# Kernel optimization log

Hardware: AMD Instinct MI355X
Metric: run time of the kernel (lower is better)

Reference implementation:

```python
import jax, jax.numpy as jnp
import numpy as np

ITER_NUM = 3       # nSteps of the SICE proximal loop (module iterNum)
NS_ITERS = 7       # Newton-Schulz iterations, hardcoded in _sice
F_LR = 5.0         # sice_lrate
F_SPARSITY = 0.07  # sparsity_val
BN_EPS = 1e-5


def _inv_sqrtm(x, iterN):
    """Batched Newton-Schulz inverse matrix square root (Sqrtm.forward)."""
    d = x.shape[-1]
    I3 = 3.0 * jnp.eye(d, dtype=x.dtype)
    normA = jnp.trace(x, axis1=-2, axis2=-1)            # [B]
    A = x / normA[:, None, None]
    ZY = 0.5 * (I3 - A)
    Y = A @ ZY
    Z = ZY
    for _ in range(iterN - 2):
        ZY = 0.5 * (I3 - Z @ Y)
        Y = Y @ ZY
        Z = ZY @ Z
    ZYZ = 0.5 * (I3 - Z @ Y) @ Z
    return ZYZ * (normA ** -0.5)[:, None, None]


def _covpool(x):
    """x: [B,C,H,W] -> centered second-order pooling [B,C,C] (Covpool)."""
    b, c, h, w = x.shape
    m = h * w
    xf = x.reshape(b, c, m)
    xc = xf - xf.mean(axis=-1, keepdims=True)
    # x @ I_hat @ x^T == (x - mean)(x - mean)^T / M
    return (xc @ xc.transpose(0, 2, 1)) / m


def _sice(x, jitter):
    C = _covpool(x)
    C = C / jnp.trace(C, axis1=-2, axis2=-1)[:, None, None]
    Ij = jnp.diag(1e-10 + 1e-9 * jitter)[None].astype(C.dtype)   # [1,D,D]
    zz = _inv_sqrtm(C + Ij, NS_ITERS)
    LLT = zz @ zz                                                # inv covariance init
    sym_C = 0.5 * (C + C.transpose(0, 2, 1))
    for i in range(ITER_NUM):
        Lp = jax.nn.relu(LLT)
        Lm = jax.nn.relu(-LLT)
        zz = _inv_sqrtm(LLT + Ij, NS_ITERS)
        g12 = -(zz @ zz) + sym_C
        dec = F_LR * (1.0 - i / (ITER_NUM - 1.0))
        Lp = jax.nn.relu(Lp - dec * (g12 + F_SPARSITY))
        Lm = jax.nn.relu(Lm - dec * (-g12 + F_SPARSITY))
        LLT = Lp - Lm
        LLT = 0.5 * (LLT + LLT.transpose(0, 2, 1))
    return LLT / jnp.sqrt(jnp.trace(LLT, axis1=-2, axis2=-1))[:, None, None]


def reference(x, conv_w, gamma, beta, jitter):
    # 1x1 conv dimension reduction + BatchNorm (batch stats, train mode) + ReLU
    y = jnp.einsum('bchw,dc->bdhw', x, conv_w)
    mu = y.mean(axis=(0, 2, 3), keepdims=True)
    var = y.var(axis=(0, 2, 3), keepdims=True)
    y = (y - mu) / jnp.sqrt(var + BN_EPS)
    y = jax.nn.relu(y * gamma[None, :, None, None] + beta[None, :, None, None])
    out = _sice(y, jitter)                                       # [B,D,D]
    b, d = out.shape[0], out.shape[1]
    iu = np.nonzero(np.triu(np.ones((d, d))).reshape(-1))[0]     # Triuvec indices
    return out.reshape(b, d * d)[:, iu]                          # [B, D*(D+1)/2]


def setup_inputs() -> dict:
    key = jax.random.key(0)
    k1, k2, k3 = jax.random.split(key, 3)
    B, CIN, H, W, DR = 32, 2048, 28, 28, 256
    x = jax.random.normal(k1, (B, CIN, H, W), dtype=jnp.float32)
    # kaiming normal, mode=fan_out (fan_out = DR*1*1): std = sqrt(2/DR)
    conv_w = jax.random.normal(k2, (DR, CIN), dtype=jnp.float32) * np.sqrt(2.0 / DR).astype(np.float32)
    gamma = jnp.ones((DR,), dtype=jnp.float32)
    beta = jnp.zeros((DR,), dtype=jnp.float32)
    jitter = jax.random.uniform(k3, (DR,), dtype=jnp.float32)
    return {"x": x, "conv_w": conv_w, "gamma": gamma, "beta": beta, "jitter": jitter}
```

## Files before the change

kernel.cpp:

```cpp
#include <hip/hip_runtime.h>
#include <utility>


typedef unsigned short u16;
typedef __attribute__((ext_vector_type(8))) __bf16 bf16x8;
typedef __attribute__((ext_vector_type(8))) _Float16 f16x8;
typedef __attribute__((ext_vector_type(4))) float f32x4;

#define DEV __device__ __forceinline__

DEV u16 f2bf(float f) {
  unsigned x = __float_as_uint(f);
  x += 0x7fffu + ((x >> 16) & 1u);
  return (u16)(x >> 16);
}
DEV float bf2f(u16 h) { return __uint_as_float(((unsigned)h) << 16); }

#define SB_SUM   0
#define SB_SSQ   256
#define SB_IJ    512
#define SB_TRC   768
#define SB_TR2   800
#define SB_TR3   832
#define SB_TRL   864
#define SB_DEN   896
#define SB_IJSUM 928

__global__ __launch_bounds__(256) void k_prep(const float* __restrict__ w,
                                              const float* __restrict__ jitter,
                                              _Float16* __restrict__ w_half,
                                              float* __restrict__ sb) {
  int gid = blockIdx.x * 256 + threadIdx.x;
  if (gid < 256 * 2048) w_half[gid] = (_Float16)w[gid];
  if (blockIdx.x == 0) {
    int t = threadIdx.x;
    sb[SB_SUM + t] = 0.f;
    sb[SB_SSQ + t] = 0.f;
    float ij = 1e-10f + 1e-9f * jitter[t];
    sb[SB_IJ + t] = ij;
    if (t < 160) sb[SB_TRC + t] = 0.f;
    __shared__ float red[256];
    red[t] = ij; __syncthreads();
    for (int off = 128; off > 0; off >>= 1) {
      if (t < off) red[t] += red[t + off];
      __syncthreads();
    }
    if (t == 0) sb[SB_IJSUM] = red[0];
  }
}

__global__ __launch_bounds__(256) void k_xt(const float* __restrict__ x,
                                            _Float16* __restrict__ xt) {
  int ht = blockIdx.x;
  int ct = blockIdx.y;
  int b = blockIdx.z;
  int t = threadIdx.x;
  __shared__ _Float16 ls[64 * 68];
  int hw0 = ht * 64, c0 = ct * 64;
  const float* xb = x + ((size_t)b * 2048 + c0) * 784;
#pragma unroll
  for (int it = 0; it < 4; ++it) {
    int cc = (t >> 4) + it * 16;
    int s = t & 15;
    int hw = hw0 + s * 4;
    float4 v = make_float4(0.f, 0.f, 0.f, 0.f);
    if (hw < 784) v = *(const float4*)(xb + (size_t)cc * 784 + hw);
    _Float16* d = &ls[cc * 68 + s * 4];
    d[0] = (_Float16)v.x; d[1] = (_Float16)v.y;
    d[2] = (_Float16)v.z; d[3] = (_Float16)v.w;
  }
  __syncthreads();
#pragma unroll
  for (int it = 0; it < 2; ++it) {
    int idx = t + it * 256;
    int hwr = idx >> 3, s8 = idx & 7;
    if (hw0 + hwr < 784) {
      union { _Float16 h[8]; uint4 v; } pk;
#pragma unroll
      for (int cc = 0; cc < 8; ++cc) pk.h[cc] = ls[(s8 * 8 + cc) * 68 + hwr];
      *(uint4*)(xt + ((size_t)b * 784 + hw0 + hwr) * 2048 + c0 + s8 * 8) = pk.v;
    }
  }
}

__global__ __launch_bounds__(256) void k_conv(const _Float16* __restrict__ w_half,
                                              const _Float16* __restrict__ xt,
                                              _Float16* __restrict__ y,
                                              float* __restrict__ sb) {
  int xb = blockIdx.x;
  int ht = xb >> 5, b = xb & 31;
  int t = threadIdx.x;
  int wv = t >> 6, lane = t & 63, m = lane & 15, quad = lane >> 4;
  __shared__ _Float16 lsA[256 * 40];
  __shared__ _Float16 lsB[32 * 40];
  int hw0 = ht * 32;
  f32x4 acc[4][2];
#pragma unroll
  for (int i = 0; i < 4; ++i)
#pragma unroll
    for (int j = 0; j < 2; ++j) acc[i][j] = (f32x4){0.f, 0.f, 0.f, 0.f};
  int rowA = t >> 2, segA = t & 3;
  const _Float16* wp = w_half + (size_t)rowA * 2048 + segA * 8;
  bool doB = (t < 128);
  int hw = hw0 + rowA;
  const _Float16* xp = xt + ((size_t)b * 784 + hw) * 2048 + segA * 8;
  uint4 ra0, ra1, ra2, ra3, rb;
  ra0 = *(const uint4*)(wp);
  ra1 = *(const uint4*)(wp + 64 * 2048);
  ra2 = *(const uint4*)(wp + 128 * 2048);
  ra3 = *(const uint4*)(wp + 192 * 2048);
  rb = (uint4){0u, 0u, 0u, 0u};
  if (doB && hw < 784) rb = *(const uint4*)(xp);
  for (int kc = 0; kc < 64; ++kc) {
    int lo = rowA * 40 + segA * 8;
    *(uint4*)&lsA[lo] = ra0;
    *(uint4*)&lsA[lo + 64 * 40] = ra1;
    *(uint4*)&lsA[lo + 128 * 40] = ra2;
    *(uint4*)&lsA[lo + 192 * 40] = ra3;
    if (doB) *(uint4*)&lsB[lo] = rb;
    __syncthreads();
    if (kc < 63) {
      int k0 = (kc + 1) * 32;
      ra0 = *(const uint4*)(wp + k0);
      ra1 = *(const uint4*)(wp + 64 * 2048 + k0);
      ra2 = *(const uint4*)(wp + 128 * 2048 + k0);
      ra3 = *(const uint4*)(wp + 192 * 2048 + k0);
      rb = (uint4){0u, 0u, 0u, 0u};
      if (doB && hw < 784) rb = *(const uint4*)(xp + k0);
    }
    f16x8 af[4], bfg[2];
#pragma unroll
    for (int i = 0; i < 4; ++i)
      af[i] = *(const f16x8*)&lsA[(wv * 64 + i * 16 + m) * 40 + quad * 8];
#pragma unroll
    for (int j = 0; j < 2; ++j)
      bfg[j] = *(const f16x8*)&lsB[(j * 16 + m) * 40 + quad * 8];
#pragma unroll
    for (int i = 0; i < 4; ++i)
#pragma unroll
      for (int j = 0; j < 2; ++j)
        acc[i][j] = __builtin_amdgcn_mfma_f32_16x16x32_f16(af[i], bfg[j], acc[i][j], 0, 0, 0);
    __syncthreads();
  }
  float* sum = sb + SB_SUM;
  float* ssq = sb + SB_SSQ;
#pragma unroll
  for (int i = 0; i < 4; ++i) {
#pragma unroll
    for (int r = 0; r < 4; ++r) {
      float s = 0.f, q = 0.f;
#pragma unroll
      for (int j = 0; j < 2; ++j) {
        float v = acc[i][j][r];
        s += v; q += v * v;
      }
      s += __shfl_xor(s, 1); s += __shfl_xor(s, 2);
      s += __shfl_xor(s, 4); s += __shfl_xor(s, 8);
      q += __shfl_xor(q, 1); q += __shfl_xor(q, 2);
      q += __shfl_xor(q, 4); q += __shfl_xor(q, 8);
      if (m == 0) {
        int R = wv * 64 + i * 16 + quad * 4 + r;
        atomicAdd(&sum[R], s);
        atomicAdd(&ssq[R], q);
      }
    }
  }
#pragma unroll
  for (int i = 0; i < 4; ++i)
#pragma unroll
    for (int j = 0; j < 2; ++j)
#pragma unroll
      for (int r = 0; r < 4; ++r) {
        int R = wv * 64 + i * 16 + quad * 4 + r;
        int hwc = hw0 + j * 16 + m;
        if (hwc < 784) y[((size_t)b * 256 + R) * 784 + hwc] = (_Float16)acc[i][j][r];
      }
}

__global__ __launch_bounds__(256) void k_bnapply(const _Float16* __restrict__ y,
                                                 const float* __restrict__ gamma,
                                                 const float* __restrict__ beta,
                                                 const float* __restrict__ sb,
                                                 _Float16* __restrict__ yc) {
  int xb = blockIdx.x;
  int d = xb >> 5, b = xb & 31, t = threadIdx.x;
  float mu = sb[SB_SUM + d] * (1.0f / 25088.0f);
  float var = sb[SB_SSQ + d] * (1.0f / 25088.0f) - mu * mu;
  float sc = gamma[d] / sqrtf(var + 1e-5f);
  float sh = beta[d] - mu * sc;
  const _Float16* row = y + ((size_t)b * 256 + d) * 784;
  float v[4];
  float s = 0.f;
#pragma unroll
  for (int i = 0; i < 4; ++i) {
    int idx = t + i * 256;
    float u = 0.f;
    if (idx < 784) u = fmaxf((float)row[idx] * sc + sh, 0.f);
    v[i] = u; s += u;
  }
  __shared__ float red[256];
  red[t] = s; __syncthreads();
  for (int off = 128; off > 0; off >>= 1) {
    if (t < off) red[t] += red[t + off];
    __syncthreads();
  }
  float mean = red[0] * (1.0f / 784.0f);
  _Float16* out = yc + ((size_t)b * 256 + d) * 800;
#pragma unroll
  for (int i = 0; i < 4; ++i) {
    int idx = t + i * 256;
    if (idx < 784) out[idx] = (_Float16)(v[i] - mean);
  }
  if (t < 16) out[784 + t] = (_Float16)0.f;
}

__global__ __launch_bounds__(256) void k_gram(const _Float16* __restrict__ yc,
                                              float* __restrict__ C,
                                              float* __restrict__ sb) {
  int xb = blockIdx.x;
  int tile = xb >> 5, b = xb & 31;
  int tr = tile >> 2, tc = tile & 3;
  int t = threadIdx.x, wv = t >> 6, lane = t & 63, m = lane & 15, quad = lane >> 4;
  int wr = (wv >> 1) * 32, wc = (wv & 1) * 32;
  __shared__ _Float16 lsA[64 * 40], lsB[64 * 40];
  f32x4 acc[2][2];
#pragma unroll
  for (int i = 0; i < 2; ++i)
#pragma unroll
    for (int j = 0; j < 2; ++j) acc[i][j] = (f32x4){0.f, 0.f, 0.f, 0.f};
  int row = t >> 2, seg = t & 3;
  const _Float16* Ap = yc + ((size_t)b * 256 + tr * 64 + row) * 800 + seg * 8;
  const _Float16* Bp = yc + ((size_t)b * 256 + tc * 64 + row) * 800 + seg * 8;
  uint4 rA = *(const uint4*)(Ap);
  uint4 rB = *(const uint4*)(Bp);
  for (int kc = 0; kc < 25; ++kc) {
    int lo = row * 40 + seg * 8;
    *(uint4*)&lsA[lo] = rA;
    *(uint4*)&lsB[lo] = rB;
    __syncthreads();
    if (kc < 24) {
      int k0 = (kc + 1) * 32;
      rA = *(const uint4*)(Ap + k0);
      rB = *(const uint4*)(Bp + k0);
    }
    f16x8 a0 = *(const f16x8*)&lsA[(wr + m) * 40 + quad * 8];
    f16x8 a1 = *(const f16x8*)&lsA[(wr + 16 + m) * 40 + quad * 8];
    f16x8 b0 = *(const f16x8*)&lsB[(wc + m) * 40 + quad * 8];
    f16x8 b1 = *(const f16x8*)&lsB[(wc + 16 + m) * 40 + quad * 8];
    acc[0][0] = __builtin_amdgcn_mfma_f32_16x16x32_f16(a0, b0, acc[0][0], 0, 0, 0);
    acc[0][1] = __builtin_amdgcn_mfma_f32_16x16x32_f16(a0, b1, acc[0][1], 0, 0, 0);
    acc[1][0] = __builtin_amdgcn_mfma_f32_16x16x32_f16(a1, b0, acc[1][0], 0, 0, 0);
    acc[1][1] = __builtin_amdgcn_mfma_f32_16x16x32_f16(a1, b1, acc[1][1], 0, 0, 0);
    __syncthreads();
  }
  const float inv = 1.0f / 784.0f;
#pragma unroll
  for (int i = 0; i < 2; ++i)
#pragma unroll
    for (int j = 0; j < 2; ++j)
#pragma unroll
      for (int r = 0; r < 4; ++r) {
        int R = tr * 64 + wr + i * 16 + quad * 4 + r;
        int Cc = tc * 64 + wc + j * 16 + m;
        float v = acc[i][j][r] * inv;
        C[((size_t)b * 256 + R) * 256 + Cc] = v;
        if (R == Cc) atomicAdd(&sb[SB_TRC + b], v);
      }
}

__global__ __launch_bounds__(256) void k_prepAZY(const float* __restrict__ src,
                                                 float* __restrict__ symC,
                                                 u16* __restrict__ Ah, u16* __restrict__ Al,
                                                 u16* __restrict__ ZYh, u16* __restrict__ ZYl,
                                                 float* __restrict__ sb, int slot, int mode) {
  int xb = blockIdx.x;
  int i = xb >> 5, b = xb & 31, j = threadIdx.x;
  float trv = (mode == 0) ? 1.0f : sb[slot + b];
  float denom = trv + sb[SB_IJSUM];
  if (i == 0 && j == 0) sb[SB_DEN + b] = denom;
  size_t idx = ((size_t)b * 256 + i) * 256 + j;
  float v;
  if (mode == 0) {
    float trC = sb[SB_TRC + b];
    float vij = src[idx] / trC;
    float vji = src[((size_t)b * 256 + j) * 256 + i] / trC;
    symC[idx] = 0.5f * (vij + vji);
    v = vij;
  } else {
    v = src[idx];
  }
  if (i == j) v += sb[SB_IJ + i];
  float A = v / denom;
  u16 h = f2bf(A);
  Ah[idx] = h; Al[idx] = f2bf(A - bf2f(h));
  float zy = 0.5f * ((i == j ? 3.0f : 0.0f) - A);
  h = f2bf(zy);
  ZYh[idx] = h; ZYl[idx] = f2bf(zy - bf2f(h));
}

struct MMArgs {
  const u16* Ah; const u16* Al; const u16* Bh; const u16* Bl;
  u16* Oh; u16* Ol; float* Of; float* tr; int emode;
};

__global__ __launch_bounds__(256) void mm_ns(MMArgs g0, MMArgs g1,
                                             const float* __restrict__ sb) {
  int xb = blockIdx.x;
  int b = xb & 31;
  int rest = xb >> 5;
  MMArgs g = (rest < 16) ? g0 : g1;
  int tile = rest & 15;
  int tr = tile >> 2, tc = tile & 3;
  int t = threadIdx.x, wv = t >> 6, lane = t & 63, m = lane & 15, quad = lane >> 4;
  int wr = (wv >> 1) * 32, wc = (wv & 1) * 32;
  __shared__ u16 lsAh[64 * 40], lsAl[64 * 40], lsBh[64 * 40], lsBl[64 * 40];
  f32x4 acc[2][2];
#pragma unroll
  for (int i = 0; i < 2; ++i)
#pragma unroll
    for (int j = 0; j < 2; ++j) acc[i][j] = (f32x4){0.f, 0.f, 0.f, 0.f};
  int row = t >> 2, seg = t & 3;
  size_t aoff = ((size_t)b * 256 + tr * 64 + row) * 256 + seg * 8;
  size_t boff = ((size_t)b * 256 + tc * 64 + row) * 256 + seg * 8;
  uint4 rAh = *(const uint4*)(g.Ah + aoff);
  uint4 rAl = *(const uint4*)(g.Al + aoff);
  uint4 rBh = *(const uint4*)(g.Bh + boff);
  uint4 rBl = *(const uint4*)(g.Bl + boff);
  for (int kc = 0; kc < 8; ++kc) {
    int lo = row * 40 + seg * 8;
    *(uint4*)&lsAh[lo] = rAh;
    *(uint4*)&lsAl[lo] = rAl;
    *(uint4*)&lsBh[lo] = rBh;
    *(uint4*)&lsBl[lo] = rBl;
    __syncthreads();
    if (kc < 7) {
      int k0 = (kc + 1) * 32;
      rAh = *(const uint4*)(g.Ah + aoff + k0);
      rAl = *(const uint4*)(g.Al + aoff + k0);
      rBh = *(const uint4*)(g.Bh + boff + k0);
      rBl = *(const uint4*)(g.Bl + boff + k0);
    }
    bf16x8 ah[2], al[2], bh[2], bl[2];
#pragma unroll
    for (int i = 0; i < 2; ++i) {
      ah[i] = *(const bf16x8*)&lsAh[(wr + i * 16 + m) * 40 + quad * 8];
      al[i] = *(const bf16x8*)&lsAl[(wr + i * 16 + m) * 40 + quad * 8];
      bh[i] = *(const bf16x8*)&lsBh[(wc + i * 16 + m) * 40 + quad * 8];
      bl[i] = *(const bf16x8*)&lsBl[(wc + i * 16 + m) * 40 + quad * 8];
    }
#pragma unroll
    for (int i = 0; i < 2; ++i)
#pragma unroll
      for (int j = 0; j < 2; ++j) {
        acc[i][j] = __builtin_amdgcn_mfma_f32_16x16x32_bf16(ah[i], bh[j], acc[i][j], 0, 0, 0);
        acc[i][j] = __builtin_amdgcn_mfma_f32_16x16x32_bf16(ah[i], bl[j], acc[i][j], 0, 0, 0);
        acc[i][j] = __builtin_amdgcn_mfma_f32_16x16x32_bf16(al[i], bh[j], acc[i][j], 0, 0, 0);
      }
    __syncthreads();
  }
  float scl = 1.0f;
  if (g.emode == 2) scl = 1.0f / sqrtf(sb[SB_DEN + b]);
#pragma unroll
  for (int i = 0; i < 2; ++i)
#pragma unroll
    for (int j = 0; j < 2; ++j)
#pragma unroll
      for (int r = 0; r < 4; ++r) {
        int R = tr * 64 + wr + i * 16 + quad * 4 + r;
        int Cc = tc * 64 + wc + j * 16 + m;
        float v = acc[i][j][r];
        if (g.emode == 1) v = 0.5f * ((R == Cc ? 3.0f : 0.0f) - v);
        else if (g.emode == 2) v = v * scl;
        size_t oidx = ((size_t)b * 256 + R) * 256 + Cc;
        if (g.emode == 3) {
          g.Of[oidx] = v;
          if (R == Cc && g.tr) atomicAdd(g.tr + b, v);
        } else {
          u16 h = f2bf(v);
          g.Oh[oidx] = h;
          g.Ol[oidx] = f2bf(v - bf2f(h));
        }
      }
}

__global__ __launch_bounds__(256) void k_sice(const float* __restrict__ LLT,
                                              const float* __restrict__ P,
                                              const float* __restrict__ symC,
                                              float* __restrict__ out,
                                              float* __restrict__ sb, int slot,
                                              float dec) {
  int xb = blockIdx.x;
  int b = xb & 31, p = xb >> 5;
  const int TRt[10] = {0, 0, 0, 0, 1, 1, 1, 2, 2, 3};
  const int TCt[10] = {0, 1, 2, 3, 1, 2, 3, 2, 3, 3};
  int tr = TRt[p], tc = TCt[p];
  __shared__ float ft[64][65];
  __shared__ float ot[64][65];
  int t = threadIdx.x;
  size_t base = (size_t)b * 65536;
#pragma unroll 4
  for (int it = 0; it < 16; ++it) {
    int idx = it * 256 + t;
    int r = idx >> 6, c = idx & 63;
    size_t o = base + (size_t)(tc * 64 + r) * 256 + tr * 64 + c;
    float L = LLT[o];
    float g = symC[o] - P[o];
    float f = fmaxf(fmaxf(L, 0.f) - dec * (g + 0.07f), 0.f) -
              fmaxf(fmaxf(-L, 0.f) - dec * (-g + 0.07f), 0.f);
    ft[r][c] = f;
  }
  __syncthreads();
  float tsum = 0.f;
#pragma unroll 4
  for (int it = 0; it < 16; ++it) {
    int idx = it * 256 + t;
    int r = idx >> 6, c = idx & 63;
    size_t o = base + (size_t)(tr * 64 + r) * 256 + tc * 64 + c;
    float L = LLT[o];
    float g = symC[o] - P[o];
    float f = fmaxf(fmaxf(L, 0.f) - dec * (g + 0.07f), 0.f) -
              fmaxf(fmaxf(-L, 0.f) - dec * (-g + 0.07f), 0.f);
    float val = 0.5f * (f + ft[c][r]);
    out[o] = val;
    ot[r][c] = val;
    if (tr == tc && r == c) tsum += val;
  }
  if (tr == tc) {
    if (tsum != 0.f) atomicAdd(&sb[slot + b], tsum);
  } else {
    __syncthreads();
#pragma unroll 4
    for (int it = 0; it < 16; ++it) {
      int idx = it * 256 + t;
      int r = idx >> 6, c = idx & 63;
      size_t o = base + (size_t)(tc * 64 + r) * 256 + tr * 64 + c;
      out[o] = ot[c][r];
    }
  }
}

__global__ __launch_bounds__(256) void k_out(const float* __restrict__ LLT,
                                             const float* __restrict__ sb,
                                             float* __restrict__ out) {
  int xb = blockIdx.x;
  int i = xb >> 5, b = xb & 31, j = threadIdx.x;
  if (j < i) return;
  float inv = 1.0f / sqrtf(sb[SB_TRL + b]);
  int tl = i * 256 - (i * (i - 1)) / 2 + (j - i);
  out[(size_t)b * 32896 + tl] = LLT[((size_t)b * 256 + i) * 256 + j] * inv;
}

extern "C" void kernel_launch(void* const* d_in, const int* in_sizes, int n_in,
                              void* d_out, int out_size, void* d_ws, size_t ws_size,
                              hipStream_t stream) {
  const float* x = (const float*)d_in[0];
  const float* w = (const float*)d_in[1];
  const float* gamma = (const float*)d_in[2];
  const float* beta = (const float*)d_in[3];
  const float* jitter = (const float*)d_in[4];
  char* ws = (char*)d_ws;

  _Float16* w_half = (_Float16*)(ws + 0);
  float* sb = (float*)(ws + (1 << 20));
  _Float16* y = (_Float16*)(ws + (2 << 20));
  _Float16* yc = (_Float16*)(ws + (16 << 20));
  _Float16* xt = (_Float16*)(ws + (32 << 20));
  char* ov = ws + (32 << 20);
  float* Craw = (float*)(ov + 0);
  float* symC = (float*)(ov + 8388608);
  float* LLTa = (float*)(ov + 16777216);
  float* P = (float*)(ov + 25165824);
  float* LLTb = (float*)(ov + 33554432);
  u16* bf[12];
  for (int i = 0; i < 12; ++i) bf[i] = (u16*)(ov + 41943040 + (size_t)i * 4194304);

  k_prep<<<2048, 256, 0, stream>>>(w, jitter, w_half, sb);
  k_xt<<<dim3(13, 32, 32), 256, 0, stream>>>(x, xt);
  k_conv<<<800, 256, 0, stream>>>(w_half, xt, y, sb);
  k_bnapply<<<8192, 256, 0, stream>>>(y, gamma, beta, sb, yc);
  k_gram<<<512, 256, 0, stream>>>(yc, Craw, sb);

  auto run_ns = [&](const float* src, int mode, int slot_in, float* Pout,
                    float* tr_out) {
    k_prepAZY<<<8192, 256, 0, stream>>>(src, symC, bf[0], bf[1], bf[2], bf[3], sb, slot_in, mode);
    u16 *Ah = bf[0], *Al = bf[1], *ZYh = bf[2], *ZYl = bf[3];
    u16 *Yh = bf[4], *Yl = bf[5], *Z2h = bf[6], *Z2l = bf[7];
    u16 *Th = bf[8], *Tl = bf[9], *zzh = bf[10], *zzl = bf[11];
    MMArgs m1{Ah, Al, ZYh, ZYl, Yh, Yl, nullptr, nullptr, 0};
    mm_ns<<<512, 256, 0, stream>>>(m1, m1, sb);
    u16 *Ych = Yh, *Ycl = Yl, *Yah = Ah, *Yal = Al;
    u16 *Zch = ZYh, *Zcl = ZYl, *Zah = Z2h, *Zal = Z2l;
    for (int it = 0; it < 5; ++it) {
      MMArgs mt{Zch, Zcl, Ych, Ycl, Th, Tl, nullptr, nullptr, 1};
      mm_ns<<<512, 256, 0, stream>>>(mt, mt, sb);
      MMArgs my{Ych, Ycl, Th, Tl, Yah, Yal, nullptr, nullptr, 0};
      MMArgs mz{Th, Tl, Zch, Zcl, Zah, Zal, nullptr, nullptr, 0};
      mm_ns<<<1024, 256, 0, stream>>>(my, mz, sb);
      std::swap(Ych, Yah); std::swap(Ycl, Yal);
      std::swap(Zch, Zah); std::swap(Zcl, Zal);
    }
    MMArgs mt6{Zch, Zcl, Ych, Ycl, Th, Tl, nullptr, nullptr, 1};
    mm_ns<<<512, 256, 0, stream>>>(mt6, mt6, sb);
    MMArgs mz7{Th, Tl, Zch, Zcl, zzh, zzl, nullptr, nullptr, 2};
    mm_ns<<<512, 256, 0, stream>>>(mz7, mz7, sb);
    MMArgs mzz{zzh, zzl, zzh, zzl, nullptr, nullptr, Pout, tr_out, 3};
    mm_ns<<<512, 256, 0, stream>>>(mzz, mzz, sb);
  };

  run_ns(Craw, 0, 0, LLTa, sb + SB_TR2);
  run_ns(LLTa, 1, SB_TR2, P, nullptr);
  k_sice<<<320, 256, 0, stream>>>(LLTa, P, symC, LLTb, sb, SB_TR3, 5.0f);
  run_ns(LLTb, 1, SB_TR3, P, nullptr);
  k_sice<<<320, 256, 0, stream>>>(LLTb, P, symC, LLTa, sb, SB_TRL, 2.5f);

  k_out<<<8192, 256, 0, stream>>>(LLTa, sb, (float*)d_out);
}
```

Measured before the change: 1.019 ms.

## Fuse input transpose into conv and drop LDS staging in gram and NS matmuls

```diff
diff --git a/kernel.cpp b/kernel.cpp
--- a/kernel.cpp
+++ b/kernel.cpp
@@ -49,92 +49,63 @@
   }
 }
 
-__global__ __launch_bounds__(256) void k_xt(const float* __restrict__ x,
-                                            _Float16* __restrict__ xt) {
-  int ht = blockIdx.x;
-  int ct = blockIdx.y;
-  int b = blockIdx.z;
-  int t = threadIdx.x;
-  __shared__ _Float16 ls[64 * 68];
-  int hw0 = ht * 64, c0 = ct * 64;
-  const float* xb = x + ((size_t)b * 2048 + c0) * 784;
-#pragma unroll
-  for (int it = 0; it < 4; ++it) {
-    int cc = (t >> 4) + it * 16;
-    int s = t & 15;
-    int hw = hw0 + s * 4;
-    float4 v = make_float4(0.f, 0.f, 0.f, 0.f);
-    if (hw < 784) v = *(const float4*)(xb + (size_t)cc * 784 + hw);
-    _Float16* d = &ls[cc * 68 + s * 4];
-    d[0] = (_Float16)v.x; d[1] = (_Float16)v.y;
-    d[2] = (_Float16)v.z; d[3] = (_Float16)v.w;
-  }
-  __syncthreads();
-#pragma unroll
-  for (int it = 0; it < 2; ++it) {
-    int idx = t + it * 256;
-    int hwr = idx >> 3, s8 = idx & 7;
-    if (hw0 + hwr < 784) {
-      union { _Float16 h[8]; uint4 v; } pk;
-#pragma unroll
-      for (int cc = 0; cc < 8; ++cc) pk.h[cc] = ls[(s8 * 8 + cc) * 68 + hwr];
-      *(uint4*)(xt + ((size_t)b * 784 + hw0 + hwr) * 2048 + c0 + s8 * 8) = pk.v;
-    }
-  }
-}
-
 __global__ __launch_bounds__(256) void k_conv(const _Float16* __restrict__ w_half,
-                                              const _Float16* __restrict__ xt,
+                                              const float* __restrict__ x,
                                               _Float16* __restrict__ y,
                                               float* __restrict__ sb) {
   int xb = blockIdx.x;
-  int ht = xb >> 5, b = xb & 31;
+  int b = xb & 31;
+  int rest = xb >> 5;
+  int mt = rest / 13, ht = rest % 13;
+  int hw0 = ht * 64;
   int t = threadIdx.x;
   int wv = t >> 6, lane = t & 63, m = lane & 15, quad = lane >> 4;
-  __shared__ _Float16 lsA[256 * 40];
-  __shared__ _Float16 lsB[32 * 40];
-  int hw0 = ht * 32;
+  __shared__ _Float16 lsA[128 * 56];
+  __shared__ _Float16 lsB[64 * 56];
   f32x4 acc[4][2];
 #pragma unroll
   for (int i = 0; i < 4; ++i)
 #pragma unroll
     for (int j = 0; j < 2; ++j) acc[i][j] = (f32x4){0.f, 0.f, 0.f, 0.f};
   int rowA = t >> 2, segA = t & 3;
-  const _Float16* wp = w_half + (size_t)rowA * 2048 + segA * 8;
-  bool doB = (t < 128);
-  int hw = hw0 + rowA;
-  const _Float16* xp = xt + ((size_t)b * 784 + hw) * 2048 + segA * 8;
-  uint4 ra0, ra1, ra2, ra3, rb;
+  const _Float16* wp = w_half + ((size_t)(mt * 128 + rowA)) * 2048 + segA * 8;
+  int hwB = lane;
+  int cg = wv;
+  bool okB = (hw0 + hwB) < 784;
+  const float* xp = x + ((size_t)b * 2048 + cg * 8) * 784 + hw0 + hwB;
+  uint4 ra0, ra1;
+  float rb[8];
   ra0 = *(const uint4*)(wp);
   ra1 = *(const uint4*)(wp + 64 * 2048);
-  ra2 = *(const uint4*)(wp + 128 * 2048);
-  ra3 = *(const uint4*)(wp + 192 * 2048);
-  rb = (uint4){0u, 0u, 0u, 0u};
-  if (doB && hw < 784) rb = *(const uint4*)(xp);
+#pragma unroll
+  for (int j = 0; j < 8; ++j) rb[j] = okB ? xp[(size_t)j * 784] : 0.f;
   for (int kc = 0; kc < 64; ++kc) {
-    int lo = rowA * 40 + segA * 8;
+    int lo = rowA * 56 + segA * 8;
     *(uint4*)&lsA[lo] = ra0;
-    *(uint4*)&lsA[lo + 64 * 40] = ra1;
-    *(uint4*)&lsA[lo + 128 * 40] = ra2;
-    *(uint4*)&lsA[lo + 192 * 40] = ra3;
-    if (doB) *(uint4*)&lsB[lo] = rb;
+    *(uint4*)&lsA[lo + 64 * 56] = ra1;
+    {
+      union { f16x8 h; uint4 u; } pk;
+#pragma unroll
+      for (int j = 0; j < 8; ++j) pk.h[j] = (_Float16)rb[j];
+      *(uint4*)&lsB[hwB * 56 + cg * 8] = pk.u;
+    }
     __syncthreads();
     if (kc < 63) {
       int k0 = (kc + 1) * 32;
       ra0 = *(const uint4*)(wp + k0);
       ra1 = *(const uint4*)(wp + 64 * 2048 + k0);
-      ra2 = *(const uint4*)(wp + 128 * 2048 + k0);
-      ra3 = *(const uint4*)(wp + 192 * 2048 + k0);
-      rb = (uint4){0u, 0u, 0u, 0u};
-      if (doB && hw < 784) rb = *(const uint4*)(xp + k0);
-    }
+#pragma unroll
+      for (int j = 0; j < 8; ++j)
+        rb[j] = okB ? xp[((size_t)k0 + j) * 784] : 0.f;
+    }
+    int wr = (wv >> 1) * 64, wc = (wv & 1) * 32;
     f16x8 af[4], bfg[2];
 #pragma unroll
     for (int i = 0; i < 4; ++i)
-      af[i] = *(const f16x8*)&lsA[(wv * 64 + i * 16 + m) * 40 + quad * 8];
+      af[i] = *(const f16x8*)&lsA[(wr + i * 16 + m) * 56 + quad * 8];
 #pragma unroll
     for (int j = 0; j < 2; ++j)
-      bfg[j] = *(const f16x8*)&lsB[(j * 16 + m) * 40 + quad * 8];
+      bfg[j] = *(const f16x8*)&lsB[(wc + j * 16 + m) * 56 + quad * 8];
 #pragma unroll
     for (int i = 0; i < 4; ++i)
 #pragma unroll
@@ -142,6 +113,7 @@
         acc[i][j] = __builtin_amdgcn_mfma_f32_16x16x32_f16(af[i], bfg[j], acc[i][j], 0, 0, 0);
     __syncthreads();
   }
+  int wr = (wv >> 1) * 64, wc = (wv & 1) * 32;
   float* sum = sb + SB_SUM;
   float* ssq = sb + SB_SSQ;
 #pragma unroll
@@ -159,7 +131,7 @@
       q += __shfl_xor(q, 1); q += __shfl_xor(q, 2);
       q += __shfl_xor(q, 4); q += __shfl_xor(q, 8);
       if (m == 0) {
-        int R = wv * 64 + i * 16 + quad * 4 + r;
+        int R = mt * 128 + wr + i * 16 + quad * 4 + r;
         atomicAdd(&sum[R], s);
         atomicAdd(&ssq[R], q);
       }
@@ -171,8 +143,8 @@
     for (int j = 0; j < 2; ++j)
 #pragma unroll
       for (int r = 0; r < 4; ++r) {
-        int R = wv * 64 + i * 16 + quad * 4 + r;
-        int hwc = hw0 + j * 16 + m;
+        int R = mt * 128 + wr + i * 16 + quad * 4 + r;
+        int hwc = hw0 + wc + j * 16 + m;
         if (hwc < 784) y[((size_t)b * 256 + R) * 784 + hwc] = (_Float16)acc[i][j][r];
       }
 }
@@ -218,54 +190,44 @@
                                               float* __restrict__ C,
                                               float* __restrict__ sb) {
   int xb = blockIdx.x;
-  int tile = xb >> 5, b = xb & 31;
-  int tr = tile >> 2, tc = tile & 3;
-  int t = threadIdx.x, wv = t >> 6, lane = t & 63, m = lane & 15, quad = lane >> 4;
-  int wr = (wv >> 1) * 32, wc = (wv & 1) * 32;
-  __shared__ _Float16 lsA[64 * 40], lsB[64 * 40];
-  f32x4 acc[2][2];
+  int b = xb & 31, rest = xb >> 5;
+  int tr = rest >> 3, tc = rest & 7;
+  int lane = threadIdx.x & 63, wv = threadIdx.x >> 6;
+  int m = lane & 15, q = lane >> 4;
+  int wr = tr * 64 + (wv >> 1) * 32;
+  int wc = tc * 32 + (wv & 1) * 16;
+  const _Float16* base = yc + (size_t)b * 256 * 800;
+  const _Float16* pa0 = base + (size_t)(wr + m) * 800 + q * 8;
+  const _Float16* pa1 = pa0 + 16 * 800;
+  const _Float16* pb = base + (size_t)(wc + m) * 800 + q * 8;
+  f32x4 acc[2];
+  acc[0] = (f32x4){0.f, 0.f, 0.f, 0.f};
+  acc[1] = (f32x4){0.f, 0.f, 0.f, 0.f};
+  f16x8 ra0 = *(const f16x8*)pa0;
+  f16x8 ra1 = *(const f16x8*)pa1;
+  f16x8 rb = *(const f16x8*)pb;
+  for (int ks = 0; ks < 25; ++ks) {
+    f16x8 ca0 = ra0, ca1 = ra1, cb = rb;
+    if (ks < 24) {
+      int k0 = (ks + 1) * 32;
+      ra0 = *(const f16x8*)(pa0 + k0);
+      ra1 = *(const f16x8*)(pa1 + k0);
+      rb = *(const f16x8*)(pb + k0);
+    }
+    acc[0] = __builtin_amdgcn_mfma_f32_16x16x32_f16(ca0, cb, acc[0], 0, 0, 0);
+    acc[1] = __builtin_amdgcn_mfma_f32_16x16x32_f16(ca1, cb, acc[1], 0, 0, 0);
+  }
+  const float inv = 1.0f / 784.0f;
 #pragma unroll
   for (int i = 0; i < 2; ++i)
 #pragma unroll
-    for (int j = 0; j < 2; ++j) acc[i][j] = (f32x4){0.f, 0.f, 0.f, 0.f};
-  int row = t >> 2, seg = t & 3;
-  const _Float16* Ap = yc + ((size_t)b * 256 + tr * 64 + row) * 800 + seg * 8;
-  const _Float16* Bp = yc + ((size_t)b * 256 + tc * 64 + row) * 800 + seg * 8;
-  uint4 rA = *(const uint4*)(Ap);
-  uint4 rB = *(const uint4*)(Bp);
-  for (int kc = 0; kc < 25; ++kc) {
-    int lo = row * 40 + seg * 8;
-    *(uint4*)&lsA[lo] = rA;
-    *(uint4*)&lsB[lo] = rB;
-    __syncthreads();
-    if (kc < 24) {
-      int k0 = (kc + 1) * 32;
-      rA = *(const uint4*)(Ap + k0);
-      rB = *(const uint4*)(Bp + k0);
-    }
-    f16x8 a0 = *(const f16x8*)&lsA[(wr + m) * 40 + quad * 8];
-    f16x8 a1 = *(const f16x8*)&lsA[(wr + 16 + m) * 40 + quad * 8];
-    f16x8 b0 = *(const f16x8*)&lsB[(wc + m) * 40 + quad * 8];
-    f16x8 b1 = *(const f16x8*)&lsB[(wc + 16 + m) * 40 + quad * 8];
-    acc[0][0] = __builtin_amdgcn_mfma_f32_16x16x32_f16(a0, b0, acc[0][0], 0, 0, 0);
-    acc[0][1] = __builtin_amdgcn_mfma_f32_16x16x32_f16(a0, b1, acc[0][1], 0, 0, 0);
-    acc[1][0] = __builtin_amdgcn_mfma_f32_16x16x32_f16(a1, b0, acc[1][0], 0, 0, 0);
-    acc[1][1] = __builtin_amdgcn_mfma_f32_16x16x32_f16(a1, b1, acc[1][1], 0, 0, 0);
-    __syncthreads();
-  }
-  const float inv = 1.0f / 784.0f;
-#pragma unroll
-  for (int i = 0; i < 2; ++i)
-#pragma unroll
-    for (int j = 0; j < 2; ++j)
-#pragma unroll
-      for (int r = 0; r < 4; ++r) {
-        int R = tr * 64 + wr + i * 16 + quad * 4 + r;
-        int Cc = tc * 64 + wc + j * 16 + m;
-        float v = acc[i][j][r] * inv;
-        C[((size_t)b * 256 + R) * 256 + Cc] = v;
-        if (R == Cc) atomicAdd(&sb[SB_TRC + b], v);
-      }
+    for (int r = 0; r < 4; ++r) {
+      int R = wr + i * 16 + q * 4 + r;
+      int Cc = wc + m;
+      float v = acc[i][r] * inv;
+      C[((size_t)b * 256 + R) * 256 + Cc] = v;
+      if (R == Cc) atomicAdd(&sb[SB_TRC + b], v);
+    }
 }
 
 __global__ __launch_bounds__(256) void k_prepAZY(const float* __restrict__ src,
@@ -308,79 +270,65 @@
   int xb = blockIdx.x;
   int b = xb & 31;
   int rest = xb >> 5;
-  MMArgs g = (rest < 16) ? g0 : g1;
-  int tile = rest & 15;
-  int tr = tile >> 2, tc = tile & 3;
-  int t = threadIdx.x, wv = t >> 6, lane = t & 63, m = lane & 15, quad = lane >> 4;
-  int wr = (wv >> 1) * 32, wc = (wv & 1) * 32;
-  __shared__ u16 lsAh[64 * 40], lsAl[64 * 40], lsBh[64 * 40], lsBl[64 * 40];
-  f32x4 acc[2][2];
-#pragma unroll
-  for (int i = 0; i < 2; ++i)
-#pragma unroll
-    for (int j = 0; j < 2; ++j) acc[i][j] = (f32x4){0.f, 0.f, 0.f, 0.f};
-  int row = t >> 2, seg = t & 3;
-  size_t aoff = ((size_t)b * 256 + tr * 64 + row) * 256 + seg * 8;
-  size_t boff = ((size_t)b * 256 + tc * 64 + row) * 256 + seg * 8;
-  uint4 rAh = *(const uint4*)(g.Ah + aoff);
-  uint4 rAl = *(const uint4*)(g.Al + aoff);
-  uint4 rBh = *(const uint4*)(g.Bh + boff);
-  uint4 rBl = *(const uint4*)(g.Bl + boff);
-  for (int kc = 0; kc < 8; ++kc) {
-    int lo = row * 40 + seg * 8;
-    *(uint4*)&lsAh[lo] = rAh;
-    *(uint4*)&lsAl[lo] = rAl;
-    *(uint4*)&lsBh[lo] = rBh;
-    *(uint4*)&lsBl[lo] = rBl;
-    __syncthreads();
-    if (kc < 7) {
-      int k0 = (kc + 1) * 32;
-      rAh = *(const uint4*)(g.Ah + aoff + k0);
-      rAl = *(const uint4*)(g.Al + aoff + k0);
-      rBh = *(const uint4*)(g.Bh + boff + k0);
-      rBl = *(const uint4*)(g.Bl + boff + k0);
-    }
-    bf16x8 ah[2], al[2], bh[2], bl[2];
-#pragma unroll
-    for (int i = 0; i < 2; ++i) {
-      ah[i] = *(const bf16x8*)&lsAh[(wr + i * 16 + m) * 40 + quad * 8];
-      al[i] = *(const bf16x8*)&lsAl[(wr + i * 16 + m) * 40 + quad * 8];
-      bh[i] = *(const bf16x8*)&lsBh[(wc + i * 16 + m) * 40 + quad * 8];
-      bl[i] = *(const bf16x8*)&lsBl[(wc + i * 16 + m) * 40 + quad * 8];
-    }
-#pragma unroll
-    for (int i = 0; i < 2; ++i)
-#pragma unroll
-      for (int j = 0; j < 2; ++j) {
-        acc[i][j] = __builtin_amdgcn_mfma_f32_16x16x32_bf16(ah[i], bh[j], acc[i][j], 0, 0, 0);
-        acc[i][j] = __builtin_amdgcn_mfma_f32_16x16x32_bf16(ah[i], bl[j], acc[i][j], 0, 0, 0);
-        acc[i][j] = __builtin_amdgcn_mfma_f32_16x16x32_bf16(al[i], bh[j], acc[i][j], 0, 0, 0);
-      }
-    __syncthreads();
+  MMArgs g = (rest < 32) ? g0 : g1;
+  int tile = rest & 31;
+  int tr = tile >> 3, tc = tile & 7;
+  int lane = threadIdx.x & 63, wv = threadIdx.x >> 6;
+  int m = lane & 15, q = lane >> 4;
+  int wr = tr * 64 + (wv >> 1) * 32;
+  int wc = tc * 32 + (wv & 1) * 16;
+  size_t mb = (size_t)b * 65536;
+  size_t a0 = mb + (size_t)(wr + m) * 256 + q * 8;
+  size_t a1 = a0 + 16 * 256;
+  size_t bo = mb + (size_t)(wc + m) * 256 + q * 8;
+  f32x4 acc[2];
+  acc[0] = (f32x4){0.f, 0.f, 0.f, 0.f};
+  acc[1] = (f32x4){0.f, 0.f, 0.f, 0.f};
+  bf16x8 ra0h = *(const bf16x8*)(g.Ah + a0);
+  bf16x8 ra1h = *(const bf16x8*)(g.Ah + a1);
+  bf16x8 ra0l = *(const bf16x8*)(g.Al + a0);
+  bf16x8 ra1l = *(const bf16x8*)(g.Al + a1);
+  bf16x8 rbh = *(const bf16x8*)(g.Bh + bo);
+  bf16x8 rbl = *(const bf16x8*)(g.Bl + bo);
+  for (int ks = 0; ks < 8; ++ks) {
+    bf16x8 ca0h = ra0h, ca1h = ra1h, ca0l = ra0l, ca1l = ra1l, cbh = rbh, cbl = rbl;
+    if (ks < 7) {
+      int k0 = (ks + 1) * 32;
+      ra0h = *(const bf16x8*)(g.Ah + a0 + k0);
+      ra1h = *(const bf16x8*)(g.Ah + a1 + k0);
+      ra0l = *(const bf16x8*)(g.Al + a0 + k0);
+      ra1l = *(const bf16x8*)(g.Al + a1 + k0);
+      rbh = *(const bf16x8*)(g.Bh + bo + k0);
+      rbl = *(const bf16x8*)(g.Bl + bo + k0);
+    }
+    acc[0] = __builtin_amdgcn_mfma_f32_16x16x32_bf16(ca0h, cbh, acc[0], 0, 0, 0);
+    acc[0] = __builtin_amdgcn_mfma_f32_16x16x32_bf16(ca0h, cbl, acc[0], 0, 0, 0);
+    acc[0] = __builtin_amdgcn_mfma_f32_16x16x32_bf16(ca0l, cbh, acc[0], 0, 0, 0);
+    acc[1] = __builtin_amdgcn_mfma_f32_16x16x32_bf16(ca1h, cbh, acc[1], 0, 0, 0);
+    acc[1] = __builtin_amdgcn_mfma_f32_16x16x32_bf16(ca1h, cbl, acc[1], 0, 0, 0);
+    acc[1] = __builtin_amdgcn_mfma_f32_16x16x32_bf16(ca1l, cbh, acc[1], 0, 0, 0);
   }
   float scl = 1.0f;
   if (g.emode == 2) scl = 1.0f / sqrtf(sb[SB_DEN + b]);
 #pragma unroll
   for (int i = 0; i < 2; ++i)
 #pragma unroll
-    for (int j = 0; j < 2; ++j)
-#pragma unroll
-      for (int r = 0; r < 4; ++r) {
-        int R = tr * 64 + wr + i * 16 + quad * 4 + r;
-        int Cc = tc * 64 + wc + j * 16 + m;
-        float v = acc[i][j][r];
-        if (g.emode == 1) v = 0.5f * ((R == Cc ? 3.0f : 0.0f) - v);
-        else if (g.emode == 2) v = v * scl;
-        size_t oidx = ((size_t)b * 256 + R) * 256 + Cc;
-        if (g.emode == 3) {
-          g.Of[oidx] = v;
-          if (R == Cc && g.tr) atomicAdd(g.tr + b, v);
-        } else {
-          u16 h = f2bf(v);
-          g.Oh[oidx] = h;
-          g.Ol[oidx] = f2bf(v - bf2f(h));
-        }
+    for (int r = 0; r < 4; ++r) {
+      int R = wr + i * 16 + q * 4 + r;
+      int Cc = wc + m;
+      float v = acc[i][r];
+      if (g.emode == 1) v = 0.5f * ((R == Cc ? 3.0f : 0.0f) - v);
+      else if (g.emode == 2) v = v * scl;
+      size_t oidx = mb + (size_t)R * 256 + Cc;
+      if (g.emode == 3) {
+        g.Of[oidx] = v;
+        if (R == Cc && g.tr) atomicAdd(g.tr + b, v);
+      } else {
+        u16 h = f2bf(v);
+        g.Oh[oidx] = h;
+        g.Ol[oidx] = f2bf(v - bf2f(h));
       }
+    }
 }
 
 __global__ __launch_bounds__(256) void k_sice(const float* __restrict__ LLT,
@@ -464,7 +412,6 @@
   float* sb = (float*)(ws + (1 << 20));
   _Float16* y = (_Float16*)(ws + (2 << 20));
   _Float16* yc = (_Float16*)(ws + (16 << 20));
-  _Float16* xt = (_Float16*)(ws + (32 << 20));
   char* ov = ws + (32 << 20);
   float* Craw = (float*)(ov + 0);
   float* symC = (float*)(ov + 8388608);
@@ -475,10 +422,9 @@
   for (int i = 0; i < 12; ++i) bf[i] = (u16*)(ov + 41943040 + (size_t)i * 4194304);
 
   k_prep<<<2048, 256, 0, stream>>>(w, jitter, w_half, sb);
-  k_xt<<<dim3(13, 32, 32), 256, 0, stream>>>(x, xt);
-  k_conv<<<800, 256, 0, stream>>>(w_half, xt, y, sb);
+  k_conv<<<832, 256, 0, stream>>>(w_half, x, y, sb);
   k_bnapply<<<8192, 256, 0, stream>>>(y, gamma, beta, sb, yc);
-  k_gram<<<512, 256, 0, stream>>>(yc, Craw, sb);
+  k_gram<<<1024, 256, 0, stream>>>(yc, Craw, sb);
 
   auto run_ns = [&](const float* src, int mode, int slot_in, float* Pout,
                     float* tr_out) {
@@ -487,24 +433,24 @@
     u16 *Yh = bf[4], *Yl = bf[5], *Z2h = bf[6], *Z2l = bf[7];
     u16 *Th = bf[8], *Tl = bf[9], *zzh = bf[10], *zzl = bf[11];
     MMArgs m1{Ah, Al, ZYh, ZYl, Yh, Yl, nullptr, nullptr, 0};
-    mm_ns<<<512, 256, 0, stream>>>(m1, m1, sb);
+    mm_ns<<<1024, 256, 0, stream>>>(m1, m1, sb);
     u16 *Ych = Yh, *Ycl = Yl, *Yah = Ah, *Yal = Al;
     u16 *Zch = ZYh, *Zcl = ZYl, *Zah = Z2h, *Zal = Z2l;
     for (int it = 0; it < 5; ++it) {
       MMArgs mt{Zch, Zcl, Ych, Ycl, Th, Tl, nullptr, nullptr, 1};
-      mm_ns<<<512, 256, 0, stream>>>(mt, mt, sb);
+      mm_ns<<<1024, 256, 0, stream>>>(mt, mt, sb);
       MMArgs my{Ych, Ycl, Th, Tl, Yah, Yal, nullptr, nullptr, 0};
       MMArgs mz{Th, Tl, Zch, Zcl, Zah, Zal, nullptr, nullptr, 0};
-      mm_ns<<<1024, 256, 0, stream>>>(my, mz, sb);
+      mm_ns<<<2048, 256, 0, stream>>>(my, mz, sb);
       std::swap(Ych, Yah); std::swap(Ycl, Yal);
       std::swap(Zch, Zah); std::swap(Zcl, Zal);
     }
     MMArgs mt6{Zch, Zcl, Ych, Ycl, Th, Tl, nullptr, nullptr, 1};
-    mm_ns<<<512, 256, 0, stream>>>(mt6, mt6, sb);
+    mm_ns<<<1024, 256, 0, stream>>>(mt6, mt6, sb);
     MMArgs mz7{Th, Tl, Zch, Zcl, zzh, zzl, nullptr, nullptr, 2};
-    mm_ns<<<512, 256, 0, stream>>>(mz7, mz7, sb);
+    mm_ns<<<1024, 256, 0, stream>>>(mz7, mz7, sb);
     MMArgs mzz{zzh, zzl, zzh, zzl, nullptr, nullptr, Pout, tr_out, 3};
-    mm_ns<<<512, 256, 0, stream>>>(mzz, mzz, sb);
+    mm_ns<<<1024, 256, 0, stream>>>(mzz, mzz, sb);
   };
 
   run_ns(Craw, 0, 0, LLTa, sb + SB_TR2);
```

After: 1.867 ms. +83.3%, slower.
